# Performance work log

Measured on AMD Instinct MI355X. Metric: run time of the kernel, lower is better.

## Reference

```python
import jax, jax.numpy as jnp
import numpy as np
from jax import lax

# QuantumDMRGLayer (isolated_labelnode=True) as a pure MPS chain contraction.
# Per sample: contract each site's (2,m[,m]) tensor with the 2-dim input vector
# over the physical leg, then multiply the resulting bond matrices along the
# chain, inserting the (m,m,nblabels) output tensor after site pos_label.

B, L, M, NBL = 2048, 196, 16, 10  # batch, dimvec, bond_len, nblabels


def setup_inputs() -> dict:
    key = jax.random.key(0)
    k_in, k_mid, k_l, k_r, k_out = jax.random.split(key, 5)
    # std chosen for numerical stability of a 196-long matrix product:
    # each site matrix is x0*A[0]+x1*A[1] with x~N(0,1), so effective per-site
    # gain ~ std*sqrt(2*m); std = 1/sqrt(2*m) keeps the product O(1).
    std = 1.0 / np.sqrt(2.0 * M)
    inputs = jax.random.normal(k_in, (B, L, 2), dtype=jnp.float32)
    eye2m = jnp.eye(M, dtype=jnp.float32)[:2, :]  # eye(max(2,m))[0:2,:] -> (2, m)
    A_left = eye2m + 1e-3 * jax.random.normal(k_l, (2, M), dtype=jnp.float32)
    A_right = eye2m + 1e-3 * jax.random.normal(k_r, (2, M), dtype=jnp.float32)
    A_mid = std * jax.random.normal(k_mid, (L - 2, 2, M, M), dtype=jnp.float32)
    T_out = (1.0 / np.sqrt(M)) * jax.random.normal(k_out, (M, M, NBL), dtype=jnp.float32)
    return {
        "inputs": inputs,
        "A_left": A_left,
        "A_mid": A_mid,
        "A_right": A_right,
        "T_out": T_out,
        "pos_label": 98,
    }


def reference(inputs, A_left, A_mid, A_right, T_out, pos_label):
    # Contract physical legs: interior site i (1..L-2) -> batched (m,m) matrix.
    mats = jnp.einsum("bsd,sdij->sbij", inputs[:, 1:-1, :], A_mid)  # (L-2, B, m, m)
    v_left = jnp.einsum("bd,dm->bm", inputs[:, 0, :], A_left)       # (B, m)
    v_right = jnp.einsum("bd,dm->bm", inputs[:, -1, :], A_right)    # (B, m)

    def step_l(v, Mx):  # v @ M, batched
        return jnp.einsum("bm,bmn->bn", v, Mx), None

    def step_r(v, Mx):  # M @ v, batched (sweep from the right end inward)
        return jnp.einsum("bmn,bn->bm", Mx, v), None

    # sites 1..pos_label feed the left bond of the output node,
    # sites pos_label+1..L-2 feed the right bond.
    left, _ = lax.scan(step_l, v_left, mats[:pos_label])
    right, _ = lax.scan(step_r, v_right, mats[pos_label:], reverse=True)
    return jnp.einsum("bm,mnl,bn->bl", left, T_out, right)  # (B, nblabels)
```

## Files before the change

kernel.cpp:

```cpp
#include <hip/hip_runtime.h>


typedef __attribute__((ext_vector_type(8))) short short8;
typedef __attribute__((ext_vector_type(16))) float floatx16;

#define GSITE_DW 512
#define GDIR_DW (100 * GSITE_DW)
#define STATE_DW (2 * GDIR_DW)

__device__ __forceinline__ unsigned bf16_rne(unsigned u) {
    return (u + 0x7FFFu + ((u >> 16) & 1u)) >> 16;
}

__global__ __launch_bounds__(256)
void prep_kernel(const float* __restrict__ AM, unsigned* __restrict__ WS)
{
    int t = blockIdx.x * 256 + threadIdx.x;
    const int w    = t & 3;  t >>= 2;
    const int lane = t & 63; t >>= 6;
    const int p    = t % 100;
    const int dir  = t / 100;
    const int kb = (lane >> 5) << 3;
    const int r  = lane & 31;
    const int rr = (r & 0x13) | ((r & 4) << 1) | ((r & 8) >> 1);
    const int d = rr >> 4, nn = rr & 15;
    const int lim = dir ? 96 : 98;
    const int a = dir ? (193 - p) : p;
    const int k0 = kb + 2 * w;
    float g0 = 0.f, g1 = 0.f;
    if (p < lim) {
        const float* Ab = AM + a * 512 + d * 256;
        if (dir == 0) { g0 = Ab[k0 * 16 + nn]; g1 = Ab[(k0 + 1) * 16 + nn]; }
        else          { g0 = Ab[nn * 16 + k0]; g1 = Ab[nn * 16 + k0 + 1]; }
    }
    const unsigned u0 = __float_as_uint(g0), u1 = __float_as_uint(g1);
    const unsigned h0 = bf16_rne(u0), h1 = bf16_rne(u1);
    const float l0f = g0 - __uint_as_float(h0 << 16);
    const float l1f = g1 - __uint_as_float(h1 << 16);
    const unsigned lo0 = bf16_rne(__float_as_uint(l0f));
    const unsigned lo1 = bf16_rne(__float_as_uint(l1f));
    unsigned* gp = WS + (dir * 100 + p) * GSITE_DW;
    gp[lane * 4 + w]       = (h1 << 16) | h0;
    gp[256 + lane * 4 + w] = (lo1 << 16) | lo0;
}

__global__ __launch_bounds__(64, 1)
void chain_kernel(const float* __restrict__ X,
                  const float* __restrict__ AL,
                  const float* __restrict__ AR,
                  const unsigned* __restrict__ WS,
                  float* __restrict__ WST)
{
    const int lane = threadIdx.x;
    const int dir  = blockIdx.x & 1;
    const int s    = (blockIdx.x >> 1) * 32 + (lane & 31);
    const int kb   = (lane >> 5) << 3;
    const float* Xs = X + s * 392;
    const unsigned* Gb = WS + dir * GDIR_DW + lane * 4;
    const int lim = dir ? 96 : 98;

    float w[8];
    int4 vh4, vl4;
    auto pack = [&]() {
#pragma unroll
        for (int q = 0; q < 4; ++q) {
            const unsigned u0 = __float_as_uint(w[2 * q]);
            const unsigned u1 = __float_as_uint(w[2 * q + 1]);
            const unsigned h0 = u0 & 0xFFFF0000u, h1 = u1 & 0xFFFF0000u;
            const float l0 = w[2 * q]     - __uint_as_float(h0);
            const float l1 = w[2 * q + 1] - __uint_as_float(h1);
            ((unsigned*)&vh4)[q] = h1 | (h0 >> 16);
            ((unsigned*)&vl4)[q] = (__float_as_uint(l1) & 0xFFFF0000u) |
                                   (__float_as_uint(l0) >> 16);
        }
    };

    const float* Ai = dir ? AR : AL;
    const float2 xi = *(const float2*)(Xs + (dir ? 390 : 0));
#pragma unroll
    for (int j = 0; j < 8; ++j)
        w[j] = xi.x * Ai[kb + j] + xi.y * Ai[16 + kb + j];
    pack();

    int4 GH[4], GL[4];
    float2 xr[4];
#pragma unroll
    for (int i = 0; i < 4; ++i) {
        GH[i] = *(const int4*)(Gb + i * GSITE_DW);
        GL[i] = *(const int4*)(Gb + i * GSITE_DW + 256);
        xr[i] = *(const float2*)(Xs + (dir ? (388 - 2 * i) : (2 + 2 * i)));
    }

    for (int c = 0; c < 25; ++c) {
#pragma unroll
        for (int j4 = 0; j4 < 4; ++j4) {
            const int p = 4 * c + j4;
            if (p < lim) {
                const short8 ah = *(short8*)&GH[j4];
                const short8 al = *(short8*)&GL[j4];
                const short8 bh = *(short8*)&vh4;
                const short8 bl = *(short8*)&vl4;
                floatx16 D = {};
                D = __builtin_amdgcn_mfma_f32_32x32x16_bf16(ah, bh, D, 0, 0, 0);
                D = __builtin_amdgcn_mfma_f32_32x32x16_bf16(ah, bl, D, 0, 0, 0);
                D = __builtin_amdgcn_mfma_f32_32x32x16_bf16(al, bh, D, 0, 0, 0);
                const float2 xs = xr[j4];
#pragma unroll
                for (int j = 0; j < 8; ++j)
                    w[j] = fmaf(xs.x, D[j], xs.y * D[j + 8]);
                pack();
            }
            const int pn = (p + 4 < 100) ? p + 4 : 99;
            GH[j4] = *(const int4*)(Gb + pn * GSITE_DW);
            GL[j4] = *(const int4*)(Gb + pn * GSITE_DW + 256);
            xr[j4] = *(const float2*)(Xs + (dir ? (388 - 2 * pn) : (2 + 2 * pn)));
        }
    }

    float* st = WST + (dir * 2048 + s) * 16 + kb;
    *(float4*)(st)     = make_float4(w[0], w[1], w[2], w[3]);
    *(float4*)(st + 4) = make_float4(w[4], w[5], w[6], w[7]);
}

__global__ __launch_bounds__(256)
void out_kernel(const float* __restrict__ T, const float* __restrict__ WST,
                float* __restrict__ OUT)
{
    __shared__ float sT[2560];
    const int tid = threadIdx.x;
    for (int k = tid; k < 640; k += 256)
        ((float4*)sT)[k] = ((const float4*)T)[k];
    __syncthreads();
    const int t = blockIdx.x * 256 + tid;
    const int s = t / 10, l = t - s * 10;
    const float* L = WST + s * 16;
    const float* R = WST + 2048 * 16 + s * 16;
    const float4 Ra = *(const float4*)(R);
    const float4 Rb = *(const float4*)(R + 4);
    const float4 Rc = *(const float4*)(R + 8);
    const float4 Rd = *(const float4*)(R + 12);
    float acc = 0.f;
#pragma unroll
    for (int m = 0; m < 16; ++m) {
        const float lm = L[m];
        const float* Tp = sT + m * 160 + l;
        acc = fmaf(lm * Ra.x, Tp[0],   acc);
        acc = fmaf(lm * Ra.y, Tp[10],  acc);
        acc = fmaf(lm * Ra.z, Tp[20],  acc);
        acc = fmaf(lm * Ra.w, Tp[30],  acc);
        acc = fmaf(lm * Rb.x, Tp[40],  acc);
        acc = fmaf(lm * Rb.y, Tp[50],  acc);
        acc = fmaf(lm * Rb.z, Tp[60],  acc);
        acc = fmaf(lm * Rb.w, Tp[70],  acc);
        acc = fmaf(lm * Rc.x, Tp[80],  acc);
        acc = fmaf(lm * Rc.y, Tp[90],  acc);
        acc = fmaf(lm * Rc.z, Tp[100], acc);
        acc = fmaf(lm * Rc.w, Tp[110], acc);
        acc = fmaf(lm * Rd.x, Tp[120], acc);
        acc = fmaf(lm * Rd.y, Tp[130], acc);
        acc = fmaf(lm * Rd.z, Tp[140], acc);
        acc = fmaf(lm * Rd.w, Tp[150], acc);
    }
    OUT[t] = acc;
}

extern "C" void kernel_launch(void* const* d_in, const int* in_sizes, int n_in,
                              void* d_out, int out_size, void* d_ws, size_t ws_size,
                              hipStream_t stream)
{
    const float* X  = (const float*)d_in[0];
    const float* AL = (const float*)d_in[1];
    const float* AM = (const float*)d_in[2];
    const float* AR = (const float*)d_in[3];
    const float* T  = (const float*)d_in[4];
    (void)in_sizes; (void)n_in; (void)out_size; (void)ws_size;
    unsigned* WS = (unsigned*)d_ws;
    float* WST   = (float*)d_ws + STATE_DW;
    float* OUT   = (float*)d_out;

    hipLaunchKernelGGL(prep_kernel,  dim3(200), dim3(256), 0, stream, AM, WS);
    hipLaunchKernelGGL(chain_kernel, dim3(128), dim3(64),  0, stream,
                       X, AL, AR, WS, WST);
    hipLaunchKernelGGL(out_kernel,   dim3(80),  dim3(256), 0, stream,
                       T, WST, OUT);
}
```

Measured before the change: 87.45 us.

## Transpose inputs in prep kernel, split MFMA accumulators, peel chain tail

The prep kernel gains extra blocks that transpose X into site-major layout, so chain-kernel lanes read coalesced float2 values per site instead of strided per-sample rows. The chain loop now runs 24 fixed iterations plus a peeled tail for the left direction, which removes the per-site bound check. The high×high MFMA goes into its own accumulator, separate from the two correction MFMAs, to shorten the dependency chain. Packing uses v_perm. The cost is an extra transpose pass over X and more prep blocks on the latency-bound serial chain.

Result: slower. 91.65 us (+4.8%).

```diff
diff --git a/kernel.cpp b/kernel.cpp
--- a/kernel.cpp
+++ b/kernel.cpp
@@ -7,46 +7,70 @@
 #define GSITE_DW 512
 #define GDIR_DW (100 * GSITE_DW)
 #define STATE_DW (2 * GDIR_DW)
+#define XT_DW (STATE_DW + 2 * 2048 * 16)
 
 __device__ __forceinline__ unsigned bf16_rne(unsigned u) {
     return (u + 0x7FFFu + ((u >> 16) & 1u)) >> 16;
 }
 
 __global__ __launch_bounds__(256)
-void prep_kernel(const float* __restrict__ AM, unsigned* __restrict__ WS)
-{
-    int t = blockIdx.x * 256 + threadIdx.x;
-    const int w    = t & 3;  t >>= 2;
-    const int lane = t & 63; t >>= 6;
-    const int p    = t % 100;
-    const int dir  = t / 100;
-    const int kb = (lane >> 5) << 3;
-    const int r  = lane & 31;
-    const int rr = (r & 0x13) | ((r & 4) << 1) | ((r & 8) >> 1);
-    const int d = rr >> 4, nn = rr & 15;
-    const int lim = dir ? 96 : 98;
-    const int a = dir ? (193 - p) : p;
-    const int k0 = kb + 2 * w;
-    float g0 = 0.f, g1 = 0.f;
-    if (p < lim) {
-        const float* Ab = AM + a * 512 + d * 256;
-        if (dir == 0) { g0 = Ab[k0 * 16 + nn]; g1 = Ab[(k0 + 1) * 16 + nn]; }
-        else          { g0 = Ab[nn * 16 + k0]; g1 = Ab[nn * 16 + k0 + 1]; }
-    }
-    const unsigned u0 = __float_as_uint(g0), u1 = __float_as_uint(g1);
-    const unsigned h0 = bf16_rne(u0), h1 = bf16_rne(u1);
-    const float l0f = g0 - __uint_as_float(h0 << 16);
-    const float l1f = g1 - __uint_as_float(h1 << 16);
-    const unsigned lo0 = bf16_rne(__float_as_uint(l0f));
-    const unsigned lo1 = bf16_rne(__float_as_uint(l1f));
-    unsigned* gp = WS + (dir * 100 + p) * GSITE_DW;
-    gp[lane * 4 + w]       = (h1 << 16) | h0;
-    gp[256 + lane * 4 + w] = (lo1 << 16) | lo0;
+void prep_kernel(const float* __restrict__ AM, const float* __restrict__ X,
+                 unsigned* __restrict__ WS)
+{
+    const int bid = blockIdx.x;
+    if (bid < 200) {
+        int t = bid * 256 + threadIdx.x;
+        const int w    = t & 3;  t >>= 2;
+        const int lane = t & 63; t >>= 6;
+        const int p    = t % 100;
+        const int dir  = t / 100;
+        const int kb = (lane >> 5) << 3;
+        const int r  = lane & 31;
+        const int rr = (r & 0x13) | ((r & 4) << 1) | ((r & 8) >> 1);
+        const int d = rr >> 4, nn = rr & 15;
+        const int lim = dir ? 96 : 98;
+        const int a = dir ? (193 - p) : p;
+        const int k0 = kb + 2 * w;
+        float g0 = 0.f, g1 = 0.f;
+        if (p < lim) {
+            const float* Ab = AM + a * 512 + d * 256;
+            if (dir == 0) { g0 = Ab[k0 * 16 + nn]; g1 = Ab[(k0 + 1) * 16 + nn]; }
+            else          { g0 = Ab[nn * 16 + k0]; g1 = Ab[nn * 16 + k0 + 1]; }
+        }
+        const unsigned h0 = bf16_rne(__float_as_uint(g0));
+        const unsigned h1 = bf16_rne(__float_as_uint(g1));
+        const float l0f = g0 - __uint_as_float(h0 << 16);
+        const float l1f = g1 - __uint_as_float(h1 << 16);
+        const unsigned lo0 = bf16_rne(__float_as_uint(l0f));
+        const unsigned lo1 = bf16_rne(__float_as_uint(l1f));
+        unsigned* gp = WS + (dir * 100 + p) * GSITE_DW;
+        gp[lane * 4 + w]       = (h1 << 16) | h0;
+        gp[256 + lane * 4 + w] = (lo1 << 16) | lo0;
+    } else {
+        __shared__ float2 tile[32][33];
+        const int q  = bid - 200;
+        const int s0 = (q & 63) * 32;
+        const int c0 = (q >> 6) * 32;
+        const int t  = threadIdx.x;
+        const int a = t & 31, b = t >> 5;
+        const float2* X2 = (const float2*)X;
+        float2* XT2 = (float2*)(WS) + (XT_DW >> 1);
+#pragma unroll
+        for (int k = 0; k < 4; ++k) {
+            const int c = c0 + a, s = s0 + b + 8 * k;
+            if (c < 196) tile[a][b + 8 * k] = X2[s * 196 + c];
+        }
+        __syncthreads();
+#pragma unroll
+        for (int k = 0; k < 4; ++k) {
+            const int c = c0 + b + 8 * k, s = s0 + a;
+            if (c < 196) XT2[c * 2048 + s] = tile[b + 8 * k][a];
+        }
+    }
 }
 
 __global__ __launch_bounds__(64, 1)
-void chain_kernel(const float* __restrict__ X,
-                  const float* __restrict__ AL,
+void chain_kernel(const float* __restrict__ AL,
                   const float* __restrict__ AR,
                   const unsigned* __restrict__ WS,
                   float* __restrict__ WST)
@@ -55,9 +79,8 @@
     const int dir  = blockIdx.x & 1;
     const int s    = (blockIdx.x >> 1) * 32 + (lane & 31);
     const int kb   = (lane >> 5) << 3;
-    const float* Xs = X + s * 392;
     const unsigned* Gb = WS + dir * GDIR_DW + lane * 4;
-    const int lim = dir ? 96 : 98;
+    const float2* Xt = (const float2*)(WS + XT_DW);
 
     float w[8];
     int4 vh4, vl4;
@@ -66,17 +89,16 @@
         for (int q = 0; q < 4; ++q) {
             const unsigned u0 = __float_as_uint(w[2 * q]);
             const unsigned u1 = __float_as_uint(w[2 * q + 1]);
-            const unsigned h0 = u0 & 0xFFFF0000u, h1 = u1 & 0xFFFF0000u;
-            const float l0 = w[2 * q]     - __uint_as_float(h0);
-            const float l1 = w[2 * q + 1] - __uint_as_float(h1);
-            ((unsigned*)&vh4)[q] = h1 | (h0 >> 16);
-            ((unsigned*)&vl4)[q] = (__float_as_uint(l1) & 0xFFFF0000u) |
-                                   (__float_as_uint(l0) >> 16);
+            const float l0 = w[2 * q]     - __uint_as_float(u0 & 0xFFFF0000u);
+            const float l1 = w[2 * q + 1] - __uint_as_float(u1 & 0xFFFF0000u);
+            ((unsigned*)&vh4)[q] = __builtin_amdgcn_perm(u1, u0, 0x07060302u);
+            ((unsigned*)&vl4)[q] = __builtin_amdgcn_perm(
+                __float_as_uint(l1), __float_as_uint(l0), 0x07060302u);
         }
     };
 
     const float* Ai = dir ? AR : AL;
-    const float2 xi = *(const float2*)(Xs + (dir ? 390 : 0));
+    const float2 xi = Xt[(dir ? 195 : 0) * 2048 + s];
 #pragma unroll
     for (int j = 0; j < 8; ++j)
         w[j] = xi.x * Ai[kb + j] + xi.y * Ai[16 + kb + j];
@@ -88,33 +110,38 @@
     for (int i = 0; i < 4; ++i) {
         GH[i] = *(const int4*)(Gb + i * GSITE_DW);
         GL[i] = *(const int4*)(Gb + i * GSITE_DW + 256);
-        xr[i] = *(const float2*)(Xs + (dir ? (388 - 2 * i) : (2 + 2 * i)));
-    }
-
-    for (int c = 0; c < 25; ++c) {
-#pragma unroll
-        for (int j4 = 0; j4 < 4; ++j4) {
-            const int p = 4 * c + j4;
-            if (p < lim) {
-                const short8 ah = *(short8*)&GH[j4];
-                const short8 al = *(short8*)&GL[j4];
-                const short8 bh = *(short8*)&vh4;
-                const short8 bl = *(short8*)&vl4;
-                floatx16 D = {};
-                D = __builtin_amdgcn_mfma_f32_32x32x16_bf16(ah, bh, D, 0, 0, 0);
-                D = __builtin_amdgcn_mfma_f32_32x32x16_bf16(ah, bl, D, 0, 0, 0);
-                D = __builtin_amdgcn_mfma_f32_32x32x16_bf16(al, bh, D, 0, 0, 0);
-                const float2 xs = xr[j4];
-#pragma unroll
-                for (int j = 0; j < 8; ++j)
-                    w[j] = fmaf(xs.x, D[j], xs.y * D[j + 8]);
-                pack();
-            }
-            const int pn = (p + 4 < 100) ? p + 4 : 99;
+        xr[i] = Xt[(dir ? (194 - i) : (1 + i)) * 2048 + s];
+    }
+
+    auto site = [&](int j4, bool pf, int pn) {
+        const short8 ah = *(short8*)&GH[j4];
+        const short8 al = *(short8*)&GL[j4];
+        const short8 bh = *(short8*)&vh4;
+        const short8 bl = *(short8*)&vl4;
+        floatx16 Da = {}, Db = {};
+        Da = __builtin_amdgcn_mfma_f32_32x32x16_bf16(ah, bh, Da, 0, 0, 0);
+        Db = __builtin_amdgcn_mfma_f32_32x32x16_bf16(ah, bl, Db, 0, 0, 0);
+        Db = __builtin_amdgcn_mfma_f32_32x32x16_bf16(al, bh, Db, 0, 0, 0);
+        const float2 xs = xr[j4];
+        if (pf) {
             GH[j4] = *(const int4*)(Gb + pn * GSITE_DW);
             GL[j4] = *(const int4*)(Gb + pn * GSITE_DW + 256);
-            xr[j4] = *(const float2*)(Xs + (dir ? (388 - 2 * pn) : (2 + 2 * pn)));
-        }
+            xr[j4] = Xt[(dir ? (194 - pn) : (1 + pn)) * 2048 + s];
+        }
+#pragma unroll
+        for (int j = 0; j < 8; ++j)
+            w[j] = fmaf(xs.x, Da[j] + Db[j], xs.y * (Da[j + 8] + Db[j + 8]));
+        pack();
+    };
+
+    for (int c = 0; c < 24; ++c) {
+#pragma unroll
+        for (int j4 = 0; j4 < 4; ++j4)
+            site(j4, true, 4 * c + j4 + 4);
+    }
+    if (dir == 0) {
+        site(0, false, 0);
+        site(1, false, 0);
     }
 
     float* st = WST + (dir * 2048 + s) * 16 + kb;
@@ -178,9 +205,9 @@
     float* WST   = (float*)d_ws + STATE_DW;
     float* OUT   = (float*)d_out;
 
-    hipLaunchKernelGGL(prep_kernel,  dim3(200), dim3(256), 0, stream, AM, WS);
+    hipLaunchKernelGGL(prep_kernel,  dim3(648), dim3(256), 0, stream, AM, X, WS);
     hipLaunchKernelGGL(chain_kernel, dim3(128), dim3(64),  0, stream,
-                       X, AL, AR, WS, WST);
+                       AL, AR, WS, WST);
     hipLaunchKernelGGL(out_kernel,   dim3(80),  dim3(256), 0, stream,
                        T, WST, OUT);
 }
```
